# Performance work log

Hardware: AMD Instinct MI355X
Metric: run time of the kernel (lower is better)

## Reference

```python
import jax, jax.numpy as jnp
import numpy as np
import math

B, T, C_IN = 4, 2048, 1024
HIDDEN, HEADS = 1024, 8
HEAD_DIM = HIDDEN // HEADS
OUT_DIM = 1024
EPS = 1e-8


def setup_inputs() -> dict:
    key = jax.random.key(0)
    ks = jax.random.split(key, 12)
    s_in = 1.0 / math.sqrt(C_IN)
    s_h = 1.0 / math.sqrt(HIDDEN)
    x = jax.random.normal(ks[0], (B, T, C_IN), dtype=jnp.float32)
    # causal keep-mask (True = keep), broadcast over batch
    attn_mask = jnp.broadcast_to(jnp.tril(jnp.ones((T, T), dtype=bool)), (B, T, T))
    Wu = jax.random.normal(ks[1], (HIDDEN, C_IN), dtype=jnp.float32) * s_in
    bu = jnp.zeros((HIDDEN,), dtype=jnp.float32)
    Wv = jax.random.normal(ks[2], (HIDDEN, C_IN), dtype=jnp.float32) * s_in
    bv = jnp.zeros((HIDDEN,), dtype=jnp.float32)
    Wq = jax.random.normal(ks[3], (HIDDEN, C_IN), dtype=jnp.float32) * s_in
    bq = jnp.zeros((HIDDEN,), dtype=jnp.float32)
    Wk = jax.random.normal(ks[4], (HIDDEN, C_IN), dtype=jnp.float32) * s_in
    bk = jnp.zeros((HIDDEN,), dtype=jnp.float32)
    Wf = jax.random.normal(ks[5], (OUT_DIM, HIDDEN), dtype=jnp.float32) * s_h
    bf = jnp.zeros((OUT_DIM,), dtype=jnp.float32)
    g_norm = jnp.ones((HIDDEN,), dtype=jnp.float32)
    return {"x": x, "attn_mask": attn_mask, "Wu": Wu, "bu": bu, "Wv": Wv,
            "bv": bv, "Wq": Wq, "bq": bq, "Wk": Wk, "bk": bk,
            "Wf": Wf, "bf": bf, "g_norm": g_norm}


def _heads(t):  # (B,T,HIDDEN) -> (B,H,T,D)
    b, s, _ = t.shape
    return t.reshape(b, s, HEADS, HEAD_DIM).transpose(0, 2, 1, 3)


def reference(x, attn_mask, Wu, bu, Wv, bv, Wq, bq, Wk, bk, Wf, bf, g_norm):
    silu = jax.nn.silu
    U = silu(x @ Wu.T + bu)
    V = silu(x @ Wv.T + bv)
    Q = silu(x @ Wq.T + bq)
    K = silu(x @ Wk.T + bk)
    Qh, Kh, Vh = _heads(Q), _heads(K), _heads(V)
    scale = 1.0 / math.sqrt(HEAD_DIM)
    logits = jnp.einsum('bhtd,bhsd->bhts', Qh, Kh) * scale
    A = jnp.maximum(silu(logits), 0.0)
    A = jnp.where(attn_mask[:, None, :, :], A, 0.0)
    denom = A.sum(axis=-1, keepdims=True)
    A = jnp.where(denom > 1e-12, A / (denom + EPS), 0.0)
    AVh = jnp.einsum('bhts,bhsd->bhtd', A, Vh)
    AV = AVh.transpose(0, 2, 1, 3).reshape(x.shape[0], x.shape[1], HIDDEN)
    # RMSNorm (torch nn.RMSNorm default eps = dtype eps)
    rms_eps = jnp.finfo(AV.dtype).eps
    AV_norm = AV * jax.lax.rsqrt(jnp.mean(AV * AV, axis=-1, keepdims=True) + rms_eps) * g_norm
    UV = AV_norm * U
    return UV @ Wf.T + bf
```

## Files before the change

### kernel.cpp

```cpp
#include <hip/hip_runtime.h>
#include <stdint.h>

#define Tlen  2048
#define M_TOK 8192

typedef __attribute__((ext_vector_type(8))) __bf16 bf16x8;
typedef __attribute__((ext_vector_type(4))) float  f32x4;
typedef unsigned short u16;
typedef unsigned int   u32;
typedef unsigned long long u64;

__device__ __forceinline__ float b2f(u16 u) {
  union { float f; u32 i; } v; v.i = ((u32)u) << 16; return v.f;
}
__device__ __forceinline__ u16 f2b(float f) {
  u32 x = __float_as_uint(f);
  return (u16)((x + 0x7FFFu + ((x >> 16) & 1u)) >> 16);
}
__device__ __forceinline__ bf16x8 ld8(const u16* p) {
  return *reinterpret_cast<const bf16x8*>(p);
}
__device__ __forceinline__ bool probe_bf16(const void* g) {
  return *(const u32*)g == 0x3F803F80u;
}
__device__ __forceinline__ void stage8(u16* dst, const void* src, size_t eidx, bool isbf) {
  if (isbf) {
    *(uint4*)dst = *(const uint4*)((const u16*)src + eidx);
  } else {
    const float* f = (const float*)src + eidx;
    float4 a = *(const float4*)f;
    float4 b = *(const float4*)(f + 4);
    u16 t[8] = { f2b(a.x), f2b(a.y), f2b(a.z), f2b(a.w),
                 f2b(b.x), f2b(b.y), f2b(b.z), f2b(b.w) };
    *(uint4*)dst = *(uint4*)t;
  }
}
__device__ __forceinline__ void gl_lds16(const void* g, void* l) {
  __builtin_amdgcn_global_load_lds(
      (const __attribute__((address_space(1))) u32*)g,
      (__attribute__((address_space(3))) u32*)l, 16, 0, 0);
}
__device__ __forceinline__ int swz128(int r, int c) {
  return r * 128 + ((((c >> 3) ^ (r & 15))) << 3) + (c & 7);
}

__global__ __launch_bounds__(256) void prep1(
    const void* __restrict__ x,
    const void* __restrict__ Wu, const void* __restrict__ Wv,
    const void* __restrict__ Wq, const void* __restrict__ Wk,
    const void* __restrict__ bu, const void* __restrict__ bv,
    const void* __restrict__ bq, const void* __restrict__ bk,
    u16* __restrict__ xb, u16* __restrict__ Wcat, u16* __restrict__ bcat,
    const void* __restrict__ gprobe)
{
  const bool isbf = probe_bf16(gprobe);
  long i = (long)blockIdx.x * 256 + threadIdx.x;
  if (i < 1048576) { stage8(&xb[i * 8], x, (size_t)i * 8, isbf); return; }
  i -= 1048576;
  if (i < 524288) {
    int w = (int)(i >> 17); long e = i & 131071;
    const void* s = (w == 0) ? Wu : (w == 1) ? Wv : (w == 2) ? Wq : Wk;
    stage8(&Wcat[((size_t)w << 20) + e * 8], s, (size_t)e * 8, isbf); return;
  }
  i -= 524288;
  if (i < 512) {
    int w = (int)(i >> 7); int e = (int)(i & 127);
    const void* s = (w == 0) ? bu : (w == 1) ? bv : (w == 2) ? bq : bk;
    stage8(&bcat[w * 1024 + e * 8], s, (size_t)e * 8, isbf);
  }
}

__global__ __launch_bounds__(256) void prep2(
    const void* __restrict__ Wf, const void* __restrict__ bf_,
    u16* __restrict__ Wfb, u16* __restrict__ bfb,
    const void* __restrict__ gprobe)
{
  const bool isbf = probe_bf16(gprobe);
  long i = (long)blockIdx.x * 256 + threadIdx.x;
  if (i < 131072) { stage8(&Wfb[i * 8], Wf, (size_t)i * 8, isbf); return; }
  i -= 131072;
  if (i < 128) stage8(&bfb[i * 8], bf_, (size_t)i * 8, isbf);
}

__global__ __launch_bounds__(256) void gemm_bf16(
    const u16* __restrict__ X,
    const u16* __restrict__ W,
    const u16* __restrict__ bias,
    void* __restrict__ O0,
    u16* __restrict__ U, u16* __restrict__ Vt,
    u16* __restrict__ Qb, u16* __restrict__ Kb,
    int mode, int apply_silu)
{
  __shared__ u16 SMEM[16384];
  u16* Xs = SMEM;
  u16* Ws = SMEM + 8192;
  const int tid  = threadIdx.x;
  const int lane = tid & 63;
  const int wave = tid >> 6;
  const int l15  = lane & 15;
  const int quad = lane >> 4;
  const int wr   = wave & 1;
  const int wc   = wave >> 1;
  const int m0 = blockIdx.y * 128;
  const int n0 = blockIdx.x * 128;

  const int ro = lane >> 3;
  const int ch = lane & 7;
  const int cc = ch ^ ro;

  f32x4 acc[4][4] = {};

  for (int k0 = 0; k0 < 1024; k0 += 64) {
    __syncthreads();
#pragma unroll
    for (int j = 0; j < 4; j++) {
      int r0 = wave * 32 + j * 8;
      gl_lds16(X + (size_t)(m0 + r0 + ro) * 1024 + k0 + cc * 8, &Xs[r0 * 64]);
      gl_lds16(W + (size_t)(n0 + r0 + ro) * 1024 + k0 + cc * 8, &Ws[r0 * 64]);
    }
    __syncthreads();

#pragma unroll
    for (int kk = 0; kk < 64; kk += 32) {
      bf16x8 a[4], b[4];
      const int g = (kk >> 3) + quad;
      const int lch = (g ^ (l15 & 7)) << 3;
#pragma unroll
      for (int mt = 0; mt < 4; mt++)
        a[mt] = ld8(&Xs[(wr * 64 + mt * 16 + l15) * 64 + lch]);
#pragma unroll
      for (int nt = 0; nt < 4; nt++)
        b[nt] = ld8(&Ws[(wc * 64 + nt * 16 + l15) * 64 + lch]);
#pragma unroll
      for (int mt = 0; mt < 4; mt++)
#pragma unroll
        for (int nt = 0; nt < 4; nt++)
          acc[mt][nt] = __builtin_amdgcn_mfma_f32_16x16x32_bf16(a[mt], b[nt], acc[mt][nt], 0, 0, 0);
    }
  }

  if (mode == 1) {
#pragma unroll
    for (int nt = 0; nt < 4; nt++) {
      int ng = n0 + wc * 64 + nt * 16 + l15;
      float bv = b2f(bias[ng]);
#pragma unroll
      for (int mt = 0; mt < 4; mt++)
#pragma unroll
        for (int r = 0; r < 4; r++) {
          int m = m0 + wr * 64 + mt * 16 + quad * 4 + r;
          ((float*)O0)[(size_t)m * 1024 + ng] = acc[mt][nt][r] + bv;
        }
    }
    return;
  }

  const int grp = blockIdx.x >> 3;
  const bool trans = (grp == 1);
  const float postmul = (grp == 3) ? 0.08838834764831845f : 1.0f;
  u16* Ls = SMEM;

  __syncthreads();
#pragma unroll
  for (int nt = 0; nt < 4; nt++) {
    int ng = n0 + wc * 64 + nt * 16 + l15;
    float bv = b2f(bias[ng]);
    int nl = wc * 64 + nt * 16 + l15;
#pragma unroll
    for (int mt = 0; mt < 4; mt++) {
#pragma unroll
      for (int r = 0; r < 4; r++) {
        int ml = wr * 64 + mt * 16 + quad * 4 + r;
        float v = acc[mt][nt][r] + bv;
        if (apply_silu) v = v * __builtin_amdgcn_rcpf(1.0f + __expf(-v));
        u16 pv = f2b(v * postmul);
        Ls[trans ? swz128(nl, ml) : swz128(ml, nl)] = pv;
      }
    }
  }
  __syncthreads();

  const int rr = tid & 127;
  const int c0 = tid >> 7;
  if (!trans) {
    u16* dst = (grp == 0) ? U : (grp == 2) ? Qb : Kb;
    const int ncol0 = (blockIdx.x & 7) * 128;
#pragma unroll
    for (int p = 0; p < 8; p++) {
      int chunk = c0 + p * 2;
      uint4 vv = *(const uint4*)&Ls[swz128(rr, chunk * 8)];
      *(uint4*)&dst[(size_t)(m0 + rr) * 1024 + ncol0 + chunk * 8] = vv;
    }
  } else {
    const int bh = (blockIdx.y >> 4) * 8 + (blockIdx.x & 7);
    const int t0 = (blockIdx.y & 15) * 128;
#pragma unroll
    for (int p = 0; p < 8; p++) {
      int chunk = c0 + p * 2;
      uint4 vv = *(const uint4*)&Ls[swz128(rr, chunk * 8)];
      *(uint4*)&Vt[((size_t)bh * 128 + rr) * 2048 + t0 + chunk * 8] = vv;
    }
  }
}

__global__ __launch_bounds__(256) void attn_kernel(
    const u16* __restrict__ Q,
    const u16* __restrict__ K,
    const u16* __restrict__ Vt,
    u16* __restrict__ AV)
{
  __shared__ u16 Ks[64 * 128];
  __shared__ u16 Vts[128 * 64];
  __shared__ u16 As[64 * 72];

  const int tid  = threadIdx.x;
  const int lane = tid & 63;
  const int wave = tid >> 6;
  const int l15  = lane & 15;
  const int quad = lane >> 4;
  const int qt = 31 - (blockIdx.x >> 5);
  const int bh = blockIdx.x & 31;
  const int q0 = qt * 64;
  const size_t rowbase = (size_t)(bh >> 3) * Tlen;
  const int cbase = (bh & 7) * 128;
  const size_t vbase = (size_t)bh * 128 * 2048;
  const int mrow = wave * 16;

  bf16x8 bq[4];
#pragma unroll
  for (int kk = 0; kk < 4; kk++)
    bq[kk] = ld8(&Q[(rowbase + q0 + mrow + l15) * 1024 + cbase + kk * 32 + quad * 8]);

  f32x4 avacc[8] = {};
  float denom = 0.f;
  const int t_abs = q0 + mrow + l15;

  for (int s0 = 0; s0 <= q0; s0 += 64) {
    __syncthreads();
    {
      const int ro16 = lane >> 4, ch16 = lane & 15;
#pragma unroll
      for (int j = 0; j < 4; j++) {
        int r0 = wave * 16 + j * 4;
        int cc = ch16 ^ ((r0 + ro16) & 15);
        gl_lds16(&K[(rowbase + s0 + r0 + ro16) * 1024 + cbase + cc * 8], &Ks[r0 * 128]);
      }
      const int ro8 = lane >> 3, ch8 = lane & 7;
#pragma unroll
      for (int j = 0; j < 4; j++) {
        int d0 = wave * 32 + j * 8;
        int cc = ch8 ^ ((d0 + ro8) & 7);
        gl_lds16(&Vt[vbase + (size_t)(d0 + ro8) * 2048 + s0 + cc * 8], &Vts[d0 * 64]);
      }
    }
    __syncthreads();

    f32x4 sacc[4] = {};
#pragma unroll
    for (int kk = 0; kk < 4; kk++) {
      bf16x8 a[4];
      const int lch = (((kk * 4) + quad) ^ l15) << 3;
#pragma unroll
      for (int nt = 0; nt < 4; nt++)
        a[nt] = ld8(&Ks[(nt * 16 + l15) * 128 + lch]);
#pragma unroll
      for (int nt = 0; nt < 4; nt++)
        sacc[nt] = __builtin_amdgcn_mfma_f32_16x16x32_bf16(a[nt], bq[kk], sacc[nt], 0, 0, 0);
    }

    const bool maskneed = (s0 + 63 > q0 + mrow);
    float rs = 0.f;
#pragma unroll
    for (int nt = 0; nt < 4; nt++) {
      u16 pk[4];
#pragma unroll
      for (int r = 0; r < 4; r++) {
        int s_abs = s0 + nt * 16 + quad * 4 + r;
        float z = sacc[nt][r];
        float aa = fmaxf(z, 0.f) * __builtin_amdgcn_rcpf(1.0f + __expf(-z));
        if (maskneed && (s_abs > t_abs)) aa = 0.0f;
        rs += aa;
        pk[r] = f2b(aa);
      }
      *(u64*)&As[(mrow + l15) * 72 + nt * 16 + quad * 4] = *(u64*)pk;
    }
    rs += __shfl_xor(rs, 16);
    rs += __shfl_xor(rs, 32);
    denom += rs;

#pragma unroll
    for (int kk = 0; kk < 2; kk++) {
      bf16x8 a, b[8];
      const int lch8 = (((kk * 4) + quad) ^ (l15 & 7)) << 3;
      a = ld8(&As[(mrow + l15) * 72 + kk * 32 + quad * 8]);
#pragma unroll
      for (int dt = 0; dt < 8; dt++)
        b[dt] = ld8(&Vts[(dt * 16 + l15) * 64 + lch8]);
#pragma unroll
      for (int dt = 0; dt < 8; dt++)
        avacc[dt] = __builtin_amdgcn_mfma_f32_16x16x32_bf16(a, b[dt], avacc[dt], 0, 0, 0);
    }
  }

  __syncthreads();
  u16* Ls = Ks;
#pragma unroll
  for (int r = 0; r < 4; r++) {
    float dn = __shfl(denom, (lane & 48) | (quad * 4 + r));
    float sc = (dn > 1e-12f) ? __builtin_amdgcn_rcpf(dn + 1e-8f) : 0.0f;
    int rl = mrow + quad * 4 + r;
#pragma unroll
    for (int dt = 0; dt < 8; dt++)
      Ls[swz128(rl, dt * 16 + l15)] = f2b(avacc[dt][r] * sc);
  }
  __syncthreads();

  const int rr = tid & 63;
  const int c0 = tid >> 6;
#pragma unroll
  for (int p = 0; p < 4; p++) {
    int chunk = c0 + p * 4;
    uint4 vv = *(const uint4*)&Ls[swz128(rr, chunk * 8)];
    *(uint4*)&AV[(rowbase + q0 + rr) * 1024 + cbase + chunk * 8] = vv;
  }
}

__global__ __launch_bounds__(256) void rms_mul(
    const u16* __restrict__ AV, const u16* __restrict__ U,
    const void* __restrict__ g, u16* __restrict__ Y)
{
  const bool isbf = probe_bf16(g);
  const int row = blockIdx.x;
  const int tid = threadIdx.x;
  const size_t base = (size_t)row * 1024;
  uint2 pav = *(const uint2*)&AV[base + tid * 4];
  const u16* pe = (const u16*)&pav;
  float v[4];
  float ss = 0.f;
#pragma unroll
  for (int j = 0; j < 4; j++) { v[j] = b2f(pe[j]); ss += v[j] * v[j]; }
#pragma unroll
  for (int m = 1; m < 64; m <<= 1) ss += __shfl_xor(ss, m);
  __shared__ float red[4];
  if ((tid & 63) == 0) red[tid >> 6] = ss;
  __syncthreads();
  float tot = red[0] + red[1] + red[2] + red[3];
  float rinv = rsqrtf(tot * (1.0f / 1024.0f) + 1.1920929e-7f);
  uint2 pu = *(const uint2*)&U[base + tid * 4];
  const u16* ue = (const u16*)&pu;
  u16 out4[4];
#pragma unroll
  for (int j = 0; j < 4; j++) {
    float gj = isbf ? b2f(((const u16*)g)[tid * 4 + j]) : ((const float*)g)[tid * 4 + j];
    out4[j] = f2b(v[j] * rinv * gj * b2f(ue[j]));
  }
  *(uint2*)&Y[base + tid * 4] = *(uint2*)out4;
}

extern "C" void kernel_launch(void* const* d_in, const int* in_sizes, int n_in,
                              void* d_out, int out_size, void* d_ws, size_t ws_size,
                              hipStream_t stream)
{
  (void)in_sizes; (void)out_size; (void)ws_size;
  const int off = (n_in >= 13) ? 0 : -1;
  const void* x   = d_in[0];
  const void* Wu  = d_in[2 + off];
  const void* bu  = d_in[3 + off];
  const void* Wv  = d_in[4 + off];
  const void* bv  = d_in[5 + off];
  const void* Wq  = d_in[6 + off];
  const void* bq  = d_in[7 + off];
  const void* Wk  = d_in[8 + off];
  const void* bk  = d_in[9 + off];
  const void* Wf  = d_in[10 + off];
  const void* bf_ = d_in[11 + off];
  const void* gn  = d_in[12 + off];

  const size_t NELT = (size_t)M_TOK * 1024;
  u16* xb  = (u16*)d_ws;
  u16* U   = xb + NELT;
  u16* Vt  = U  + NELT;
  u16* Qb  = Vt + NELT;
  u16* Kb  = Qb + NELT;
  u16* AVb = Qb;
  u16* Y   = Kb;
  u16* Wfb = xb;
  u16* bfb = xb + (size_t)1024 * 1024;

  u16* Wcat = (u16*)d_out;
  u16* bcat = Wcat + (size_t)4096 * 1024;

  prep1<<<dim3(6146), 256, 0, stream>>>(x, Wu, Wv, Wq, Wk, bu, bv, bq, bk,
                                        xb, Wcat, bcat, gn);

  gemm_bf16<<<dim3(32, 64), 256, 0, stream>>>(xb, Wcat, bcat, nullptr,
                                              U, Vt, Qb, Kb, 2, 1);

  prep2<<<dim3(513), 256, 0, stream>>>(Wf, bf_, Wfb, bfb, gn);

  attn_kernel<<<dim3(1024), 256, 0, stream>>>(Qb, Kb, Vt, AVb);
  rms_mul<<<dim3(M_TOK), 256, 0, stream>>>(AVb, U, gn, Y);

  gemm_bf16<<<dim3(8, 64), 256, 0, stream>>>(Y, Wfb, bfb, d_out,
                                             nullptr, nullptr, nullptr, nullptr, 1, 0);
}
```

Before: 362.6 us.

## Write non-transposed projection outputs directly and alias attention score buffer onto K tile

The projection epilogue for U, Q and K now writes bf16 values straight from registers to global memory, skipping the LDS staging round-trip. Only the V path keeps the transpose through shared memory. In the attention kernel the score buffer now reuses the K tile's shared memory, with an extra barrier added after the QK product, and launch bounds request 4 blocks per CU. The goal is less LDS traffic and footprint so occupancy can rise. The cost is scattered 2-byte global stores in place of 16-byte vector stores, plus an added barrier.

```diff
diff --git a/kernel.cpp b/kernel.cpp
--- a/kernel.cpp
+++ b/kernel.cpp
@@ -156,10 +156,30 @@
   }
 
   const int grp = blockIdx.x >> 3;
-  const bool trans = (grp == 1);
-  const float postmul = (grp == 3) ? 0.08838834764831845f : 1.0f;
+
+  if (grp != 1) {
+    u16* dst = (grp == 0) ? U : (grp == 2) ? Qb : Kb;
+    const float postmul = (grp == 3) ? 0.08838834764831845f : 1.0f;
+#pragma unroll
+    for (int nt = 0; nt < 4; nt++) {
+      int ng = n0 + wc * 64 + nt * 16 + l15;
+      float bv = b2f(bias[ng]);
+      int ncol = ng & 1023;
+#pragma unroll
+      for (int mt = 0; mt < 4; mt++) {
+#pragma unroll
+        for (int r = 0; r < 4; r++) {
+          int m = m0 + wr * 64 + mt * 16 + quad * 4 + r;
+          float v = acc[mt][nt][r] + bv;
+          if (apply_silu) v = v * __builtin_amdgcn_rcpf(1.0f + __expf(-v));
+          dst[(size_t)m * 1024 + ncol] = f2b(v * postmul);
+        }
+      }
+    }
+    return;
+  }
+
   u16* Ls = SMEM;
-
   __syncthreads();
 #pragma unroll
   for (int nt = 0; nt < 4; nt++) {
@@ -173,8 +193,7 @@
         int ml = wr * 64 + mt * 16 + quad * 4 + r;
         float v = acc[mt][nt][r] + bv;
         if (apply_silu) v = v * __builtin_amdgcn_rcpf(1.0f + __expf(-v));
-        u16 pv = f2b(v * postmul);
-        Ls[trans ? swz128(nl, ml) : swz128(ml, nl)] = pv;
+        Ls[swz128(nl, ml)] = f2b(v);
       }
     }
   }
@@ -182,28 +201,17 @@
 
   const int rr = tid & 127;
   const int c0 = tid >> 7;
-  if (!trans) {
-    u16* dst = (grp == 0) ? U : (grp == 2) ? Qb : Kb;
-    const int ncol0 = (blockIdx.x & 7) * 128;
-#pragma unroll
-    for (int p = 0; p < 8; p++) {
-      int chunk = c0 + p * 2;
-      uint4 vv = *(const uint4*)&Ls[swz128(rr, chunk * 8)];
-      *(uint4*)&dst[(size_t)(m0 + rr) * 1024 + ncol0 + chunk * 8] = vv;
-    }
-  } else {
-    const int bh = (blockIdx.y >> 4) * 8 + (blockIdx.x & 7);
-    const int t0 = (blockIdx.y & 15) * 128;
-#pragma unroll
-    for (int p = 0; p < 8; p++) {
-      int chunk = c0 + p * 2;
-      uint4 vv = *(const uint4*)&Ls[swz128(rr, chunk * 8)];
-      *(uint4*)&Vt[((size_t)bh * 128 + rr) * 2048 + t0 + chunk * 8] = vv;
-    }
-  }
-}
-
-__global__ __launch_bounds__(256) void attn_kernel(
+  const int bh = (blockIdx.y >> 4) * 8 + (blockIdx.x & 7);
+  const int t0 = (blockIdx.y & 15) * 128;
+#pragma unroll
+  for (int p = 0; p < 8; p++) {
+    int chunk = c0 + p * 2;
+    uint4 vv = *(const uint4*)&Ls[swz128(rr, chunk * 8)];
+    *(uint4*)&Vt[((size_t)bh * 128 + rr) * 2048 + t0 + chunk * 8] = vv;
+  }
+}
+
+__global__ __launch_bounds__(256, 4) void attn_kernel(
     const u16* __restrict__ Q,
     const u16* __restrict__ K,
     const u16* __restrict__ Vt,
@@ -211,7 +219,7 @@
 {
   __shared__ u16 Ks[64 * 128];
   __shared__ u16 Vts[128 * 64];
-  __shared__ u16 As[64 * 72];
+  u16* As = Ks;
 
   const int tid  = threadIdx.x;
   const int lane = tid & 63;
@@ -267,6 +275,7 @@
       for (int nt = 0; nt < 4; nt++)
         sacc[nt] = __builtin_amdgcn_mfma_f32_16x16x32_bf16(a[nt], bq[kk], sacc[nt], 0, 0, 0);
     }
+    __syncthreads();
 
     const bool maskneed = (s0 + 63 > q0 + mrow);
     float rs = 0.f;
```

After: 355.6 us. About the same (-1.9%).
